# Performance work log

Hardware: AMD Instinct MI355X
Metric: run time of the kernel (lower is better)

## Reference

```python
import jax, jax.numpy as jnp
import numpy as np

N_NODES = 50000
N_EDGES = 1_600_000
IN_FEATS = 256
N_HEADS = 2
OUT_FEATS = 64
NEG_SLOPE = 0.2


def setup_inputs() -> dict:
    key = jax.random.key(0)
    k1, k2, k3, k4, k5, k6 = jax.random.split(key, 6)
    feat = jax.random.normal(k1, (N_NODES, IN_FEATS), dtype=jnp.float32)
    src = jax.random.randint(k2, (N_EDGES,), 0, N_NODES, dtype=jnp.int32)
    dst = jax.random.randint(k3, (N_EDGES,), 0, N_NODES, dtype=jnp.int32)
    W = jax.random.normal(k4, (IN_FEATS, N_HEADS * OUT_FEATS), dtype=jnp.float32) * 0.05
    attn_l = jax.random.normal(k5, (N_HEADS, OUT_FEATS), dtype=jnp.float32) * 0.1
    attn_r = jax.random.normal(k6, (N_HEADS, OUT_FEATS), dtype=jnp.float32) * 0.1
    return {"feat": feat, "src": src, "dst": dst, "W": W, "attn_l": attn_l, "attn_r": attn_r}


def reference(feat, src, dst, W, attn_l, attn_r):
    # node projection: [N, H, F]
    ft = (feat @ W).reshape(N_NODES, N_HEADS, OUT_FEATS)
    el = jnp.einsum('nhf,hf->nh', ft, attn_l)  # [N, H]
    er = jnp.einsum('nhf,hf->nh', ft, attn_r)  # [N, H]
    # per-edge logits + leaky relu
    e = el[src] + er[dst]                      # [E, H]
    e = jnp.where(e > 0, e, NEG_SLOPE * e)
    # segment softmax over incoming edges of each dst node
    m = jax.ops.segment_max(e, dst, num_segments=N_NODES)     # [N, H]
    m = jnp.where(jnp.isfinite(m), m, 0.0)                     # guard empty segments
    e_exp = jnp.exp(e - jax.lax.stop_gradient(m)[dst])         # [E, H]
    s = jax.ops.segment_sum(e_exp, dst, num_segments=N_NODES)  # [N, H]
    a = e_exp / jnp.maximum(s[dst], 1e-20)                     # [E, H]
    # scatter-weighted aggregation: sum_e a_e * ft[src_e] into dst
    msg = ft[src] * a[:, :, None]                              # [E, H, F]
    rst = jax.ops.segment_sum(msg, dst, num_segments=N_NODES)  # [N, H, F]
    return rst
```

## Files before the change

kernel.cpp:

```cpp
#include <hip/hip_runtime.h>
#include <hip/hip_fp16.h>

#define N_NODES 50000
#define N_EDGES 1600000
#define IN_F 256
#define NEG_SLOPE 0.2f
#define CHUNK 1024
#define NCH ((N_NODES + CHUNK - 1) / CHUNK)

__global__ __launch_bounds__(256) void k_gemm(const float* __restrict__ feat,
                                              const float* __restrict__ W,
                                              const float* __restrict__ attn_l,
                                              const float* __restrict__ attn_r,
                                              __half* __restrict__ ft16,
                                              float* __restrict__ el,
                                              float* __restrict__ er) {
  __shared__ __align__(16) float Wl[32 * 128];
  __shared__ __align__(16) float Fl[64 * 33];
  const int tid = threadIdx.x;
  const int cg = tid & 15;
  const int rg = tid >> 4;
  const int col0 = cg * 8, rowt = rg * 4;
  const int row0 = blockIdx.x * 64;
  float acc[4][8];
#pragma unroll
  for (int i = 0; i < 4; ++i)
#pragma unroll
    for (int j = 0; j < 8; ++j) acc[i][j] = 0.f;

  for (int kt = 0; kt < IN_F; kt += 32) {
    __syncthreads();
#pragma unroll
    for (int j = 0; j < 4; ++j) {
      int idx = tid + j * 256;
      ((float4*)Wl)[idx] = ((const float4*)(W + kt * 128))[idx];
    }
#pragma unroll
    for (int j = 0; j < 2; ++j) {
      int r = j * 32 + (tid >> 3);
      int kk = (tid & 7) * 4;
      int grow = row0 + r;
      if (grow >= N_NODES) grow = N_NODES - 1;
      float4 v = *(const float4*)(feat + (size_t)grow * IN_F + kt + kk);
      float* fp = &Fl[r * 33 + kk];
      fp[0] = v.x; fp[1] = v.y; fp[2] = v.z; fp[3] = v.w;
    }
    __syncthreads();
#pragma unroll
    for (int k = 0; k < 32; ++k) {
      float4 w0 = *(const float4*)&Wl[k * 128 + col0];
      float4 w1 = *(const float4*)&Wl[k * 128 + col0 + 4];
#pragma unroll
      for (int i = 0; i < 4; ++i) {
        float f = Fl[(rowt + i) * 33 + k];
        acc[i][0] = fmaf(f, w0.x, acc[i][0]);
        acc[i][1] = fmaf(f, w0.y, acc[i][1]);
        acc[i][2] = fmaf(f, w0.z, acc[i][2]);
        acc[i][3] = fmaf(f, w0.w, acc[i][3]);
        acc[i][4] = fmaf(f, w1.x, acc[i][4]);
        acc[i][5] = fmaf(f, w1.y, acc[i][5]);
        acc[i][6] = fmaf(f, w1.z, acc[i][6]);
        acc[i][7] = fmaf(f, w1.w, acc[i][7]);
      }
    }
  }
  float al[8], ar[8];
#pragma unroll
  for (int j = 0; j < 8; ++j) { al[j] = attn_l[col0 + j]; ar[j] = attn_r[col0 + j]; }
#pragma unroll
  for (int i = 0; i < 4; ++i) {
    int row = row0 + rowt + i;
    float sl = 0.f, sr = 0.f;
#pragma unroll
    for (int j = 0; j < 8; ++j) { sl = fmaf(acc[i][j], al[j], sl); sr = fmaf(acc[i][j], ar[j], sr); }
#pragma unroll
    for (int m = 1; m < 8; m <<= 1) { sl += __shfl_xor(sl, m, 64); sr += __shfl_xor(sr, m, 64); }
    if (row < N_NODES) {
      __half2 h0 = __floats2half2_rn(acc[i][0], acc[i][1]);
      __half2 h1 = __floats2half2_rn(acc[i][2], acc[i][3]);
      __half2 h2 = __floats2half2_rn(acc[i][4], acc[i][5]);
      __half2 h3 = __floats2half2_rn(acc[i][6], acc[i][7]);
      uint4 pk = make_uint4(*(unsigned*)&h0, *(unsigned*)&h1,
                            *(unsigned*)&h2, *(unsigned*)&h3);
      *(uint4*)(ft16 + (size_t)row * 128 + col0) = pk;
      if ((cg & 7) == 0) {
        int h = cg >> 3;
        el[row * 2 + h] = sl;
        er[row * 2 + h] = sr;
      }
    }
  }
}

__global__ __launch_bounds__(256) void k_deg(const int* __restrict__ dst,
                                             int* __restrict__ deg,
                                             ushort* __restrict__ rank) {
  int t = blockIdx.x * 256 + threadIdx.x;
  if (t >= N_EDGES / 4) return;
  int4 d4 = ((const int4*)dst)[t];
  ushort4 r;
  r.x = (ushort)atomicAdd(&deg[d4.x], 1);
  r.y = (ushort)atomicAdd(&deg[d4.y], 1);
  r.z = (ushort)atomicAdd(&deg[d4.z], 1);
  r.w = (ushort)atomicAdd(&deg[d4.w], 1);
  ((ushort4*)rank)[t] = r;
}

__global__ __launch_bounds__(256) void k_scanA(const int* __restrict__ deg,
                                               int* __restrict__ csum) {
  __shared__ int ws[4];
  int b = blockIdx.x, tid = threadIdx.x, lane = tid & 63, w = tid >> 6;
  int i0 = b * CHUNK + tid * 4;
  int s = 0;
#pragma unroll
  for (int j = 0; j < 4; ++j) {
    int i = i0 + j;
    if (i < N_NODES) s += deg[i];
  }
#pragma unroll
  for (int m = 32; m > 0; m >>= 1) s += __shfl_xor(s, m, 64);
  if (lane == 0) ws[w] = s;
  __syncthreads();
  if (tid == 0) csum[b] = ws[0] + ws[1] + ws[2] + ws[3];
}

__global__ void k_scanB(const int* __restrict__ csum, int* __restrict__ coff,
                        int* __restrict__ rowptr) {
  int tid = threadIdx.x;
  int v = (tid < NCH) ? csum[tid] : 0;
  int x = v;
#pragma unroll
  for (int off = 1; off < 64; off <<= 1) {
    int y = __shfl_up(x, off, 64);
    if (tid >= off) x += y;
  }
  if (tid < NCH) coff[tid] = x - v;
  if (tid == NCH - 1) rowptr[N_NODES] = x;
}

__global__ __launch_bounds__(256) void k_scanC(const int* __restrict__ deg,
                                               const int* __restrict__ coff,
                                               int* __restrict__ rowptr) {
  __shared__ int wtot[4];
  int b = blockIdx.x, tid = threadIdx.x, lane = tid & 63, w = tid >> 6;
  int i0 = b * CHUNK + tid * 4;
  int d[4];
#pragma unroll
  for (int j = 0; j < 4; ++j) d[j] = (i0 + j < N_NODES) ? deg[i0 + j] : 0;
  int t1 = d[0] + d[1], t2 = t1 + d[2], t3 = t2 + d[3];
  int x = t3;
#pragma unroll
  for (int off = 1; off < 64; off <<= 1) {
    int y = __shfl_up(x, off, 64);
    if (lane >= off) x += y;
  }
  if (lane == 63) wtot[w] = x;
  __syncthreads();
  int woff = 0;
  for (int j = 0; j < w; ++j) woff += wtot[j];
  int excl = coff[b] + woff + (x - t3);
  int pre[4] = {0, d[0], t1, t2};
#pragma unroll
  for (int j = 0; j < 4; ++j) {
    int i = i0 + j;
    if (i < N_NODES) rowptr[i] = excl + pre[j];
  }
}

__device__ __forceinline__ void sort1(int s, int d, int rk,
                                      const int* __restrict__ rowptr,
                                      const float2* __restrict__ el2,
                                      const float2* __restrict__ er2,
                                      unsigned long long* __restrict__ rec) {
  float2 a = el2[s];
  float2 b = er2[d];
  float e0 = a.x + b.x, e1 = a.y + b.y;
  e0 = e0 > 0.f ? e0 : NEG_SLOPE * e0;
  e1 = e1 > 0.f ? e1 : NEG_SLOPE * e1;
  __half2 h = __floats2half2_rn(__expf(e0), __expf(e1));
  unsigned long long v =
      ((unsigned long long)(*(unsigned*)&h) << 32) | (unsigned)s;
  rec[rowptr[d] + rk] = v;
}

__global__ __launch_bounds__(256) void k_sortp(const int* __restrict__ src,
                                               const int* __restrict__ dst,
                                               const ushort* __restrict__ rank,
                                               const int* __restrict__ rowptr,
                                               const float2* __restrict__ el2,
                                               const float2* __restrict__ er2,
                                               unsigned long long* __restrict__ rec) {
  int t = blockIdx.x * 256 + threadIdx.x;
  if (t >= N_EDGES / 4) return;
  int4 s4 = ((const int4*)src)[t];
  int4 d4 = ((const int4*)dst)[t];
  ushort4 r4 = ((const ushort4*)rank)[t];
  sort1(s4.x, d4.x, r4.x, rowptr, el2, er2, rec);
  sort1(s4.y, d4.y, r4.y, rowptr, el2, er2, rec);
  sort1(s4.z, d4.z, r4.z, rowptr, el2, er2, rec);
  sort1(s4.w, d4.w, r4.w, rowptr, el2, er2, rec);
}

__global__ __launch_bounds__(256) void k_agg(const unsigned long long* __restrict__ rec,
                                             const int* __restrict__ rowptr,
                                             const __half2* __restrict__ ft2,
                                             float2* __restrict__ out) {
  int t = blockIdx.x * 256 + threadIdx.x;
  int node = t >> 6, lane = t & 63;
  if (node >= N_NODES) return;
  int beg = rowptr[node], end = rowptr[node + 1];
  bool h1 = lane >= 32;
  float ax = 0.f, ay = 0.f, s = 0.f;
  int i = beg;
  for (; i + 8 <= end; i += 8) {
    unsigned long long r[8];
#pragma unroll
    for (int j = 0; j < 8; ++j) r[j] = __builtin_nontemporal_load(&rec[i + j]);
    __half2 f[8];
#pragma unroll
    for (int j = 0; j < 8; ++j)
      f[j] = ft2[(size_t)(unsigned)(r[j] & 0xffffffffu) * 64 + lane];
#pragma unroll
    for (int j = 0; j < 8; ++j) {
      unsigned pw = (unsigned)(r[j] >> 32);
      float2 p = __half22float2(*(const __half2*)&pw);
      float a = h1 ? p.y : p.x;
      float2 g = __half22float2(f[j]);
      ax = fmaf(a, g.x, ax); ay = fmaf(a, g.y, ay);
      s += a;
    }
  }
  for (; i < end; ++i) {
    unsigned long long r = rec[i];
    unsigned pw = (unsigned)(r >> 32);
    float2 p = __half22float2(*(const __half2*)&pw);
    float a = h1 ? p.y : p.x;
    float2 g = __half22float2(ft2[(size_t)(unsigned)(r & 0xffffffffu) * 64 + lane]);
    ax = fmaf(a, g.x, ax); ay = fmaf(a, g.y, ay);
    s += a;
  }
  float inv = 1.f / fmaxf(s, 1e-20f);
  out[(size_t)node * 64 + lane] = make_float2(ax * inv, ay * inv);
}

extern "C" void kernel_launch(void* const* d_in, const int* in_sizes, int n_in,
                              void* d_out, int out_size, void* d_ws, size_t ws_size,
                              hipStream_t stream) {
  const float* feat   = (const float*)d_in[0];
  const int*   src    = (const int*)d_in[1];
  const int*   dst    = (const int*)d_in[2];
  const float* W      = (const float*)d_in[3];
  const float* attn_l = (const float*)d_in[4];
  const float* attn_r = (const float*)d_in[5];
  float* out = (float*)d_out;

  char* base = (char*)d_ws;
  size_t off = 0;
  auto bump = [&](size_t bytes) -> void* {
    void* p = base + off;
    off = (off + bytes + 255) & ~(size_t)255;
    return p;
  };
  __half* ft16   = (__half*)bump(sizeof(__half) * N_NODES * 128);
  float*  el     = (float*)bump(sizeof(float) * N_NODES * 2);
  float*  er     = (float*)bump(sizeof(float) * N_NODES * 2);
  int*    deg    = (int*)bump(sizeof(int) * N_NODES);
  int*    csum   = (int*)bump(sizeof(int) * NCH);
  int*    coff   = (int*)bump(sizeof(int) * NCH);
  int*    rowptr = (int*)bump(sizeof(int) * (N_NODES + 1));
  ushort* rank   = (ushort*)bump(sizeof(ushort) * N_EDGES);
  unsigned long long* rec =
      (unsigned long long*)bump(sizeof(unsigned long long) * N_EDGES);
  (void)ws_size; (void)in_sizes; (void)n_in; (void)out_size;

  (void)hipMemsetAsync(deg, 0, sizeof(int) * N_NODES, stream);

  k_deg<<<(N_EDGES / 4 + 255) / 256, 256, 0, stream>>>(dst, deg, rank);
  k_gemm<<<(N_NODES + 63) / 64, 256, 0, stream>>>(feat, W, attn_l, attn_r, ft16, el, er);
  k_scanA<<<NCH, 256, 0, stream>>>(deg, csum);
  k_scanB<<<1, 64, 0, stream>>>(csum, coff, rowptr);
  k_scanC<<<NCH, 256, 0, stream>>>(deg, coff, rowptr);
  k_sortp<<<(N_EDGES / 4 + 255) / 256, 256, 0, stream>>>(src, dst, rank, rowptr,
      (const float2*)el, (const float2*)er, rec);
  k_agg<<<(N_NODES * 64 + 255) / 256, 256, 0, stream>>>(rec, rowptr,
      (const __half2*)ft16, (float2*)out);
}
```

Baseline: 327.1 us.

## Use MFMA fp16 GEMM and privatize degree counters into eight copies

After: 301.8 us. 7.7% less time.

```diff
diff --git a/kernel.cpp b/kernel.cpp
--- a/kernel.cpp
+++ b/kernel.cpp
@@ -7,6 +7,11 @@
 #define NEG_SLOPE 0.2f
 #define CHUNK 1024
 #define NCH ((N_NODES + CHUNK - 1) / CHUNK)
+#define NPAD 50048
+#define NCOPY 8
+
+typedef _Float16 f16x8 __attribute__((ext_vector_type(8)));
+typedef float f32x4 __attribute__((ext_vector_type(4)));
 
 __global__ __launch_bounds__(256) void k_gemm(const float* __restrict__ feat,
                                               const float* __restrict__ W,
@@ -15,107 +20,125 @@
                                               __half* __restrict__ ft16,
                                               float* __restrict__ el,
                                               float* __restrict__ er) {
-  __shared__ __align__(16) float Wl[32 * 128];
-  __shared__ __align__(16) float Fl[64 * 33];
+  __shared__ __align__(16) _Float16 Wt[4 * 128 * 8];
+  __shared__ __align__(16) _Float16 Fl[64 * 40];
   const int tid = threadIdx.x;
-  const int cg = tid & 15;
-  const int rg = tid >> 4;
-  const int col0 = cg * 8, rowt = rg * 4;
+  const int lane = tid & 63;
+  const int w = tid >> 6;
+  const int c0 = lane & 15;
+  const int g = lane >> 4;
   const int row0 = blockIdx.x * 64;
-  float acc[4][8];
-#pragma unroll
-  for (int i = 0; i < 4; ++i)
-#pragma unroll
-    for (int j = 0; j < 8; ++j) acc[i][j] = 0.f;
+
+  f32x4 acc[8];
+#pragma unroll
+  for (int t = 0; t < 8; ++t) acc[t] = f32x4{0.f, 0.f, 0.f, 0.f};
+
+  const int fr = tid >> 2;
+  const int fk = (tid & 3) * 8;
+  const int wc = tid & 127;
+  const int wgp = tid >> 7;
 
   for (int kt = 0; kt < IN_F; kt += 32) {
     __syncthreads();
-#pragma unroll
-    for (int j = 0; j < 4; ++j) {
-      int idx = tid + j * 256;
-      ((float4*)Wl)[idx] = ((const float4*)(W + kt * 128))[idx];
-    }
-#pragma unroll
-    for (int j = 0; j < 2; ++j) {
-      int r = j * 32 + (tid >> 3);
-      int kk = (tid & 7) * 4;
-      int grow = row0 + r;
+    {
+      int grow = row0 + fr;
       if (grow >= N_NODES) grow = N_NODES - 1;
-      float4 v = *(const float4*)(feat + (size_t)grow * IN_F + kt + kk);
-      float* fp = &Fl[r * 33 + kk];
-      fp[0] = v.x; fp[1] = v.y; fp[2] = v.z; fp[3] = v.w;
+      const float* fp = feat + (size_t)grow * IN_F + kt + fk;
+      float4 v0 = *(const float4*)fp;
+      float4 v1 = *(const float4*)(fp + 4);
+      f16x8 h;
+      h[0] = (_Float16)v0.x; h[1] = (_Float16)v0.y;
+      h[2] = (_Float16)v0.z; h[3] = (_Float16)v0.w;
+      h[4] = (_Float16)v1.x; h[5] = (_Float16)v1.y;
+      h[6] = (_Float16)v1.z; h[7] = (_Float16)v1.w;
+      *(f16x8*)&Fl[fr * 40 + fk] = h;
+    }
+#pragma unroll
+    for (int gg = 0; gg < 2; ++gg) {
+      int gw = wgp * 2 + gg;
+      f16x8 h;
+#pragma unroll
+      for (int j = 0; j < 8; ++j)
+        h[j] = (_Float16)W[(size_t)(kt + gw * 8 + j) * 128 + wc];
+      *(f16x8*)&Wt[(gw * 128 + wc) * 8] = h;
     }
     __syncthreads();
-#pragma unroll
-    for (int k = 0; k < 32; ++k) {
-      float4 w0 = *(const float4*)&Wl[k * 128 + col0];
-      float4 w1 = *(const float4*)&Wl[k * 128 + col0 + 4];
-#pragma unroll
-      for (int i = 0; i < 4; ++i) {
-        float f = Fl[(rowt + i) * 33 + k];
-        acc[i][0] = fmaf(f, w0.x, acc[i][0]);
-        acc[i][1] = fmaf(f, w0.y, acc[i][1]);
-        acc[i][2] = fmaf(f, w0.z, acc[i][2]);
-        acc[i][3] = fmaf(f, w0.w, acc[i][3]);
-        acc[i][4] = fmaf(f, w1.x, acc[i][4]);
-        acc[i][5] = fmaf(f, w1.y, acc[i][5]);
-        acc[i][6] = fmaf(f, w1.z, acc[i][6]);
-        acc[i][7] = fmaf(f, w1.w, acc[i][7]);
+    f16x8 a = *(const f16x8*)&Fl[(w * 16 + c0) * 40 + g * 8];
+#pragma unroll
+    for (int t = 0; t < 8; ++t) {
+      f16x8 b = *(const f16x8*)&Wt[(g * 128 + t * 16 + c0) * 8];
+      acc[t] = __builtin_amdgcn_mfma_f32_16x16x32_f16(a, b, acc[t], 0, 0, 0);
+    }
+  }
+
+  float al8[8], ar8[8];
+#pragma unroll
+  for (int t = 0; t < 8; ++t) {
+    al8[t] = attn_l[t * 16 + c0];
+    ar8[t] = attn_r[t * 16 + c0];
+  }
+#pragma unroll
+  for (int r = 0; r < 4; ++r) {
+    int row = row0 + w * 16 + g * 4 + r;
+    float sl0 = 0.f, sl1 = 0.f, sr0 = 0.f, sr1 = 0.f;
+#pragma unroll
+    for (int t = 0; t < 4; ++t) {
+      sl0 = fmaf(acc[t][r], al8[t], sl0);
+      sr0 = fmaf(acc[t][r], ar8[t], sr0);
+    }
+#pragma unroll
+    for (int t = 4; t < 8; ++t) {
+      sl1 = fmaf(acc[t][r], al8[t], sl1);
+      sr1 = fmaf(acc[t][r], ar8[t], sr1);
+    }
+#pragma unroll
+    for (int m = 1; m < 16; m <<= 1) {
+      sl0 += __shfl_xor(sl0, m, 64);
+      sl1 += __shfl_xor(sl1, m, 64);
+      sr0 += __shfl_xor(sr0, m, 64);
+      sr1 += __shfl_xor(sr1, m, 64);
+    }
+    if (row < N_NODES) {
+#pragma unroll
+      for (int t = 0; t < 8; ++t)
+        ft16[(size_t)row * 128 + t * 16 + c0] = __float2half(acc[t][r]);
+      if (c0 == 0) {
+        el[row * 2 + 0] = sl0; el[row * 2 + 1] = sl1;
+        er[row * 2 + 0] = sr0; er[row * 2 + 1] = sr1;
       }
     }
   }
-  float al[8], ar[8];
-#pragma unroll
-  for (int j = 0; j < 8; ++j) { al[j] = attn_l[col0 + j]; ar[j] = attn_r[col0 + j]; }
-#pragma unroll
-  for (int i = 0; i < 4; ++i) {
-    int row = row0 + rowt + i;
-    float sl = 0.f, sr = 0.f;
-#pragma unroll
-    for (int j = 0; j < 8; ++j) { sl = fmaf(acc[i][j], al[j], sl); sr = fmaf(acc[i][j], ar[j], sr); }
-#pragma unroll
-    for (int m = 1; m < 8; m <<= 1) { sl += __shfl_xor(sl, m, 64); sr += __shfl_xor(sr, m, 64); }
-    if (row < N_NODES) {
-      __half2 h0 = __floats2half2_rn(acc[i][0], acc[i][1]);
-      __half2 h1 = __floats2half2_rn(acc[i][2], acc[i][3]);
-      __half2 h2 = __floats2half2_rn(acc[i][4], acc[i][5]);
-      __half2 h3 = __floats2half2_rn(acc[i][6], acc[i][7]);
-      uint4 pk = make_uint4(*(unsigned*)&h0, *(unsigned*)&h1,
-                            *(unsigned*)&h2, *(unsigned*)&h3);
-      *(uint4*)(ft16 + (size_t)row * 128 + col0) = pk;
-      if ((cg & 7) == 0) {
-        int h = cg >> 3;
-        el[row * 2 + h] = sl;
-        er[row * 2 + h] = sr;
-      }
-    }
-  }
 }
 
 __global__ __launch_bounds__(256) void k_deg(const int* __restrict__ dst,
-                                             int* __restrict__ deg,
+                                             int* __restrict__ deg8,
                                              ushort* __restrict__ rank) {
   int t = blockIdx.x * 256 + threadIdx.x;
   if (t >= N_EDGES / 4) return;
+  int* mydeg = deg8 + (blockIdx.x & 7) * NPAD;
   int4 d4 = ((const int4*)dst)[t];
   ushort4 r;
-  r.x = (ushort)atomicAdd(&deg[d4.x], 1);
-  r.y = (ushort)atomicAdd(&deg[d4.y], 1);
-  r.z = (ushort)atomicAdd(&deg[d4.z], 1);
-  r.w = (ushort)atomicAdd(&deg[d4.w], 1);
+  r.x = (ushort)atomicAdd(&mydeg[d4.x], 1);
+  r.y = (ushort)atomicAdd(&mydeg[d4.y], 1);
+  r.z = (ushort)atomicAdd(&mydeg[d4.z], 1);
+  r.w = (ushort)atomicAdd(&mydeg[d4.w], 1);
   ((ushort4*)rank)[t] = r;
 }
 
-__global__ __launch_bounds__(256) void k_scanA(const int* __restrict__ deg,
+__global__ __launch_bounds__(256) void k_scanA(const int* __restrict__ deg8,
                                                int* __restrict__ csum) {
   __shared__ int ws[4];
   int b = blockIdx.x, tid = threadIdx.x, lane = tid & 63, w = tid >> 6;
   int i0 = b * CHUNK + tid * 4;
   int s = 0;
 #pragma unroll
-  for (int j = 0; j < 4; ++j) {
-    int i = i0 + j;
-    if (i < N_NODES) s += deg[i];
+  for (int c = 0; c < NCOPY; ++c) {
+    const int* dp = deg8 + c * NPAD;
+#pragma unroll
+    for (int j = 0; j < 4; ++j) {
+      int i = i0 + j;
+      if (i < N_NODES) s += dp[i];
+    }
   }
 #pragma unroll
   for (int m = 32; m > 0; m >>= 1) s += __shfl_xor(s, m, 64);
@@ -138,15 +161,20 @@
   if (tid == NCH - 1) rowptr[N_NODES] = x;
 }
 
-__global__ __launch_bounds__(256) void k_scanC(const int* __restrict__ deg,
+__global__ __launch_bounds__(256) void k_scanC(const int* __restrict__ deg8,
                                                const int* __restrict__ coff,
                                                int* __restrict__ rowptr) {
   __shared__ int wtot[4];
   int b = blockIdx.x, tid = threadIdx.x, lane = tid & 63, w = tid >> 6;
   int i0 = b * CHUNK + tid * 4;
-  int d[4];
-#pragma unroll
-  for (int j = 0; j < 4; ++j) d[j] = (i0 + j < N_NODES) ? deg[i0 + j] : 0;
+  int d[4] = {0, 0, 0, 0};
+#pragma unroll
+  for (int c = 0; c < NCOPY; ++c) {
+    const int* dp = deg8 + c * NPAD;
+#pragma unroll
+    for (int j = 0; j < 4; ++j)
+      if (i0 + j < N_NODES) d[j] += dp[i0 + j];
+  }
   int t1 = d[0] + d[1], t2 = t1 + d[2], t3 = t2 + d[3];
   int x = t3;
 #pragma unroll
@@ -167,8 +195,21 @@
   }
 }
 
+__global__ __launch_bounds__(256) void k_off8(const int* __restrict__ deg8,
+                                              const int* __restrict__ rowptr,
+                                              int* __restrict__ off8) {
+  int d = blockIdx.x * 256 + threadIdx.x;
+  if (d >= N_NODES) return;
+  int run = rowptr[d];
+#pragma unroll
+  for (int c = 0; c < NCOPY; ++c) {
+    off8[c * NPAD + d] = run;
+    run += deg8[c * NPAD + d];
+  }
+}
+
 __device__ __forceinline__ void sort1(int s, int d, int rk,
-                                      const int* __restrict__ rowptr,
+                                      const int* __restrict__ myoff,
                                       const float2* __restrict__ el2,
                                       const float2* __restrict__ er2,
                                       unsigned long long* __restrict__ rec) {
@@ -180,25 +221,26 @@
   __half2 h = __floats2half2_rn(__expf(e0), __expf(e1));
   unsigned long long v =
       ((unsigned long long)(*(unsigned*)&h) << 32) | (unsigned)s;
-  rec[rowptr[d] + rk] = v;
+  rec[myoff[d] + rk] = v;
 }
 
 __global__ __launch_bounds__(256) void k_sortp(const int* __restrict__ src,
                                                const int* __restrict__ dst,
                                                const ushort* __restrict__ rank,
-                                               const int* __restrict__ rowptr,
+                                               const int* __restrict__ off8,
                                                const float2* __restrict__ el2,
                                                const float2* __restrict__ er2,
                                                unsigned long long* __restrict__ rec) {
   int t = blockIdx.x * 256 + threadIdx.x;
   if (t >= N_EDGES / 4) return;
+  const int* myoff = off8 + (blockIdx.x & 7) * NPAD;
   int4 s4 = ((const int4*)src)[t];
   int4 d4 = ((const int4*)dst)[t];
   ushort4 r4 = ((const ushort4*)rank)[t];
-  sort1(s4.x, d4.x, r4.x, rowptr, el2, er2, rec);
-  sort1(s4.y, d4.y, r4.y, rowptr, el2, er2, rec);
-  sort1(s4.z, d4.z, r4.z, rowptr, el2, er2, rec);
-  sort1(s4.w, d4.w, r4.w, rowptr, el2, er2, rec);
+  sort1(s4.x, d4.x, r4.x, myoff, el2, er2, rec);
+  sort1(s4.y, d4.y, r4.y, myoff, el2, er2, rec);
+  sort1(s4.z, d4.z, r4.z, myoff, el2, er2, rec);
+  sort1(s4.w, d4.w, r4.w, myoff, el2, er2, rec);
 }
 
 __global__ __launch_bounds__(256) void k_agg(const unsigned long long* __restrict__ rec,
@@ -264,7 +306,8 @@
   __half* ft16   = (__half*)bump(sizeof(__half) * N_NODES * 128);
   float*  el     = (float*)bump(sizeof(float) * N_NODES * 2);
   float*  er     = (float*)bump(sizeof(float) * N_NODES * 2);
-  int*    deg    = (int*)bump(sizeof(int) * N_NODES);
+  int*    deg8   = (int*)bump(sizeof(int) * NCOPY * NPAD);
+  int*    off8   = (int*)bump(sizeof(int) * NCOPY * NPAD);
   int*    csum   = (int*)bump(sizeof(int) * NCH);
   int*    coff   = (int*)bump(sizeof(int) * NCH);
   int*    rowptr = (int*)bump(sizeof(int) * (N_NODES + 1));
@@ -273,14 +316,15 @@
       (unsigned long long*)bump(sizeof(unsigned long long) * N_EDGES);
   (void)ws_size; (void)in_sizes; (void)n_in; (void)out_size;
 
-  (void)hipMemsetAsync(deg, 0, sizeof(int) * N_NODES, stream);
-
-  k_deg<<<(N_EDGES / 4 + 255) / 256, 256, 0, stream>>>(dst, deg, rank);
+  (void)hipMemsetAsync(deg8, 0, sizeof(int) * NCOPY * NPAD, stream);
+
+  k_deg<<<(N_EDGES / 4 + 255) / 256, 256, 0, stream>>>(dst, deg8, rank);
   k_gemm<<<(N_NODES + 63) / 64, 256, 0, stream>>>(feat, W, attn_l, attn_r, ft16, el, er);
-  k_scanA<<<NCH, 256, 0, stream>>>(deg, csum);
+  k_scanA<<<NCH, 256, 0, stream>>>(deg8, csum);
   k_scanB<<<1, 64, 0, stream>>>(csum, coff, rowptr);
-  k_scanC<<<NCH, 256, 0, stream>>>(deg, coff, rowptr);
-  k_sortp<<<(N_EDGES / 4 + 255) / 256, 256, 0, stream>>>(src, dst, rank, rowptr,
+  k_scanC<<<NCH, 256, 0, stream>>>(deg8, coff, rowptr);
+  k_off8<<<(N_NODES + 255) / 256, 256, 0, stream>>>(deg8, rowptr, off8);
+  k_sortp<<<(N_EDGES / 4 + 255) / 256, 256, 0, stream>>>(src, dst, rank, off8,
       (const float2*)el, (const float2*)er, rec);
   k_agg<<<(N_NODES * 64 + 255) / 256, 256, 0, stream>>>(rec, rowptr,
       (const __half2*)ft16, (float2*)out);
```
